# Optimization experiments

Measured on AMD Instinct MI355X. Metric: run time of the kernel, lower is better.

The kernel has to match this reference:

```python
import jax, jax.numpy as jnp
import numpy as np

INF = 10000.0


def setup_inputs() -> dict:
    key = jax.random.key(0)
    ks = jax.random.split(key, 4)
    bs, seqlen, hidden = 8, 512, 768
    head_size, heads = 64, 12
    inputs = jax.random.normal(ks[0], (bs, seqlen, hidden), dtype=jnp.float32)
    attention_mask = jnp.ones((bs, seqlen), dtype=jnp.int32)
    W1 = jax.random.normal(ks[1], (hidden, head_size * 2), dtype=jnp.float32) * 0.02
    b1 = jnp.zeros((head_size * 2,), dtype=jnp.float32)
    W2 = jax.random.normal(ks[2], (head_size * 2, heads * 2), dtype=jnp.float32) * 0.02
    b2 = jnp.zeros((heads * 2,), dtype=jnp.float32)
    return {"inputs": inputs, "attention_mask": attention_mask,
            "W1": W1, "b1": b1, "W2": W2, "b2": b2}


def _rope(t, sin, cos):
    # t: [b, s, d]; sin/cos: [s, d//2]
    t1, t2 = t[..., 0::2], t[..., 1::2]
    return jnp.stack([t1 * cos - t2 * sin, t1 * sin + t2 * cos], axis=-1).reshape(t.shape)


def reference(inputs, attention_mask, W1, b1, W2, b2):
    bs, seqlen = inputs.shape[:2]
    head_size = W1.shape[1] // 2
    x = inputs @ W1 + b1                      # [b, s, 2*head_size]
    qw, kw = x[..., 0::2], x[..., 1::2]       # [b, s, head_size] each
    # rotary embedding (computed like the buffer in the torch module)
    pos = jnp.arange(seqlen, dtype=jnp.float32)
    inv_freq = 1.0 / (10000.0 ** (jnp.arange(0, head_size, 2, dtype=jnp.float32) / head_size))
    freqs = pos[:, None] * inv_freq[None, :]  # [s, head_size//2]
    sin, cos = jnp.sin(freqs), jnp.cos(freqs)
    qw = _rope(qw, sin, cos)
    kw = _rope(kw, sin, cos)
    logits = jnp.einsum('bmd,bnd->bmn', qw, kw) / (head_size ** 0.5)  # [b, s, s]
    bias = (x @ W2 + b2).transpose(0, 2, 1) / 2.0                      # [b, 2*heads, s]
    logits = logits[:, None] + bias[:, ::2, None, :] + bias[:, 1::2, :, None]  # [b, h, s, s]
    am = attention_mask.astype(logits.dtype)
    mask = 1.0 - am[:, None, None, :] * am[:, None, :, None]           # [b, 1, s, s]
    logits = logits - mask * INF
    # tril mask: positions with end < start (j < i)
    idx = jnp.arange(seqlen)
    tril = (idx[None, :] < idx[:, None]).astype(logits.dtype)[None, None]  # [1, 1, s, s]
    logits = logits - tril * INF
    mask_out = jnp.logical_or(mask.astype(bool),
                              jnp.broadcast_to(tril.astype(bool), (bs, 1, seqlen, seqlen)))
    return logits, mask_out
```

## Files before the change

kernel.cpp:

```cpp
#include <hip/hip_runtime.h>

#define BSZ 8
#define SEQ 512
#define HID 768
#define N1 128
#define N2 24
#define HS 64
#define HEADS 12
#define INFV 10000.0f

typedef __attribute__((ext_vector_type(8))) short s8b;
typedef __attribute__((ext_vector_type(4))) float f32x4;

__device__ __forceinline__ unsigned short f2bf(float f) {
    union { float f; unsigned int u; } c; c.f = f;
    unsigned int u = c.u;
    u += 0x7FFFu + ((u >> 16) & 1u);
    return (unsigned short)(u >> 16);
}

__global__ __launch_bounds__(128) void k0_w1t(const float* __restrict__ W1,
                                              unsigned short* __restrict__ W1T) {
    const int c = threadIdx.x;
    const int k0 = blockIdx.x * 8;
    unsigned short v[8];
#pragma unroll
    for (int i = 0; i < 8; ++i)
        v[i] = f2bf(W1[(size_t)(k0 + i) * N1 + c]);
    unsigned short* dst = W1T + (size_t)c * HID + k0;
#pragma unroll
    for (int i = 0; i < 8; ++i) dst[i] = v[i];
}

__global__ __launch_bounds__(512, 2) void k1_proj(
    const float* __restrict__ inp, const unsigned short* __restrict__ W1T,
    const float* __restrict__ b1, const float* __restrict__ W2,
    const float* __restrict__ b2, float* __restrict__ qw,
    float* __restrict__ kwT, float* __restrict__ biasT)
{
    __shared__ unsigned short aF[96 * 16 * 8];
    __shared__ float xs[16 * N1];
    __shared__ float kT[HS][17];

    const int tid = threadIdx.x;
    const int row0 = blockIdx.x * 16;
    const int b = row0 >> 9;
    const int m0 = row0 & 511;

    {
        const float4* src = (const float4*)(inp + (size_t)row0 * HID);
#pragma unroll
        for (int i = 0; i < 6; ++i) {
            int f4 = tid + i * 512;
            int r = f4 / 192;
            int c4 = f4 % 192;
            float4 v = src[f4];
            int chunk = c4 >> 1;
            int half = c4 & 1;
            ushort4 w;
            w.x = f2bf(v.x); w.y = f2bf(v.y); w.z = f2bf(v.z); w.w = f2bf(v.w);
            *(ushort4*)&aF[(chunk * 16 + r) * 8 + half * 4] = w;
        }
    }
    __syncthreads();

    const int wv = tid >> 6;
    const int ln = tid & 63;
    const int lr = ln & 15;
    const int lg = ln >> 4;
    const int c0 = wv * 16;

    const s8b* bp = (const s8b*)W1T + ((size_t)(c0 + lr) * 96 + lg);

    f32x4 acc = {0.f, 0.f, 0.f, 0.f};
#pragma unroll
    for (int kc = 0; kc < 24; ++kc) {
        s8b a = *(const s8b*)&aF[((kc * 4 + lg) * 16 + lr) * 8];
        s8b bw = bp[kc * 4];
        acc = __builtin_amdgcn_mfma_f32_16x16x32_bf16(a, bw, acc, 0, 0, 0);
    }

    {
        float b1v = b1[c0 + lr];
#pragma unroll
        for (int g = 0; g < 4; ++g)
            xs[(lg * 4 + g) * N1 + c0 + lr] = acc[g] + b1v;
    }
    __syncthreads();

    {
        const int r = tid >> 5, j = tid & 31;
        const int m = m0 + r;
        const float C = 0.4152410118609203f;
        float invf = exp2f(-(float)j * C);
        float ang = (float)m * invf;
        float sv, cv;
        sincosf(ang, &sv, &cv);
        float4 xv = *(const float4*)&xs[r * N1 + 4 * j];
        float rq0 = xv.x * cv - xv.z * sv;
        float rq1 = xv.x * sv + xv.z * cv;
        float rk0 = xv.y * cv - xv.w * sv;
        float rk1 = xv.y * sv + xv.w * cv;
        *(float2*)(qw + (size_t)(b * SEQ + m) * HS + 2 * j) = make_float2(rq0, rq1);
        kT[2 * j][r]     = rk0;
        kT[2 * j + 1][r] = rk1;
    }
    if (tid < 16 * N2) {
        int r = tid / N2, c = tid - r * N2;
        const float* xr = &xs[r * N1];
        float dot = b2[c];
#pragma unroll 8
        for (int k = 0; k < N1; ++k)
            dot = fmaf(xr[k], W2[k * N2 + c], dot);
        biasT[(size_t)(b * N2 + c) * SEQ + m0 + r] = dot * 0.5f;
    }
    __syncthreads();

    {
        int d = tid >> 3, q = tid & 7;
        float2 v = *(const float2*)&kT[d][2 * q];
        *(float2*)(kwT + (size_t)(b * HS + d) * SEQ + m0 + 2 * q) = v;
    }
}

__global__ __launch_bounds__(256) void k2_out(
    const float* __restrict__ qw, const float* __restrict__ kwT,
    const float* __restrict__ biasT, const int* __restrict__ am,
    float* __restrict__ out)
{
    __shared__ float q_lds[8][HS];
    __shared__ float bo[8][HEADS];
    __shared__ int amm[8];

    const int tid = threadIdx.x;
    const int b = blockIdx.x >> 6;
    const int m0 = (blockIdx.x & 63) * 8;

#pragma unroll
    for (int i = 0; i < 2; ++i) {
        int idx = tid + i * 256;
        q_lds[idx >> 6][idx & 63] = qw[(size_t)(b * SEQ + m0) * HS + idx];
    }
    if (tid < 96) {
        int r = tid / 12, h = tid - r * 12;
        bo[r][h] = biasT[(size_t)(b * N2 + 2 * h + 1) * SEQ + m0 + r];
    }
    if (tid < 8) amm[tid] = am[b * SEQ + m0 + tid];
    __syncthreads();

    const int n0 = tid * 2;
    float qk0[8] = {0, 0, 0, 0, 0, 0, 0, 0};
    float qk1[8] = {0, 0, 0, 0, 0, 0, 0, 0};

#pragma unroll
    for (int dc = 0; dc < 2; ++dc) {
        float2 kn[32];
#pragma unroll
        for (int d = 0; d < 32; ++d)
            kn[d] = *(const float2*)&kwT[(size_t)(b * HS + dc * 32 + d) * SEQ + n0];
#pragma unroll
        for (int r = 0; r < 8; ++r) {
#pragma unroll
            for (int d4 = 0; d4 < 8; ++d4) {
                float4 qv = *(const float4*)&q_lds[r][dc * 32 + d4 * 4];
                qk0[r] = fmaf(qv.x, kn[d4 * 4 + 0].x, qk0[r]);
                qk0[r] = fmaf(qv.y, kn[d4 * 4 + 1].x, qk0[r]);
                qk0[r] = fmaf(qv.z, kn[d4 * 4 + 2].x, qk0[r]);
                qk0[r] = fmaf(qv.w, kn[d4 * 4 + 3].x, qk0[r]);
                qk1[r] = fmaf(qv.x, kn[d4 * 4 + 0].y, qk1[r]);
                qk1[r] = fmaf(qv.y, kn[d4 * 4 + 1].y, qk1[r]);
                qk1[r] = fmaf(qv.z, kn[d4 * 4 + 2].y, qk1[r]);
                qk1[r] = fmaf(qv.w, kn[d4 * 4 + 3].y, qk1[r]);
            }
        }
    }

    const int amn0 = am[b * SEQ + n0];
    const int amn1 = am[b * SEQ + n0 + 1];
    float pen0[8], pen1[8];
    float2 mo[8];
#pragma unroll
    for (int r = 0; r < 8; ++r) {
        int m = m0 + r;
        float msk0 = (1.0f - (float)(amn0 * amm[r])) * INFV;
        float msk1 = (1.0f - (float)(amn1 * amm[r])) * INFV;
        pen0[r] = msk0 + ((n0 < m) ? INFV : 0.0f);
        pen1[r] = msk1 + ((n0 + 1 < m) ? INFV : 0.0f);
        bool b0 = (amn0 * amm[r] != 1) || (n0 < m);
        bool b1m = (amn1 * amm[r] != 1) || (n0 + 1 < m);
        mo[r].x = b0 ? 1.0f : 0.0f;
        mo[r].y = b1m ? 1.0f : 0.0f;
    }

    float2 be[HEADS];
#pragma unroll
    for (int h = 0; h < HEADS; ++h)
        be[h] = *(const float2*)&biasT[(size_t)(b * N2 + 2 * h) * SEQ + n0];

    const size_t obase = (size_t)b * HEADS * SEQ * SEQ + n0;
#pragma unroll
    for (int h = 0; h < HEADS; ++h) {
#pragma unroll
        for (int r = 0; r < 8; ++r) {
            float2 v;
            v.x = fmaf(qk0[r], 0.125f, be[h].x + bo[r][h]) - pen0[r];
            v.y = fmaf(qk1[r], 0.125f, be[h].y + bo[r][h]) - pen1[r];
            *(float2*)&out[obase + ((size_t)h * SEQ + m0 + r) * SEQ] = v;
        }
    }
    const size_t mbase = (size_t)BSZ * HEADS * SEQ * SEQ
                       + ((size_t)b * SEQ + m0) * SEQ + n0;
#pragma unroll
    for (int r = 0; r < 8; ++r)
        *(float2*)&out[mbase + (size_t)r * SEQ] = mo[r];
}

extern "C" void kernel_launch(void* const* d_in, const int* in_sizes, int n_in,
                              void* d_out, int out_size, void* d_ws, size_t ws_size,
                              hipStream_t stream) {
    const float* inp = (const float*)d_in[0];
    const int*   am  = (const int*)d_in[1];
    const float* W1  = (const float*)d_in[2];
    const float* b1  = (const float*)d_in[3];
    const float* W2  = (const float*)d_in[4];
    const float* b2  = (const float*)d_in[5];

    float* ws    = (float*)d_ws;
    float* qw    = ws;
    float* kwT   = ws + 262144;
    float* biasT = ws + 524288;
    unsigned short* W1T = (unsigned short*)(ws + 622592);

    float* out = (float*)d_out;

    hipLaunchKernelGGL(k0_w1t, dim3(96), dim3(128), 0, stream, W1, W1T);
    hipLaunchKernelGGL(k1_proj, dim3(4096 / 16), dim3(512), 0, stream,
                       inp, W1T, b1, W2, b2, qw, kwT, biasT);
    hipLaunchKernelGGL(k2_out, dim3(4096 / 8), dim3(256), 0, stream,
                       qw, kwT, biasT, am, out);
}
```

Before: 48.23 us.

## Split projection kernel over column halves and precompute rope and W2 transpose

The projection kernel now runs twice as many blocks, each covering half of the 128 output columns. Within a block, the K dimension is split across two wave groups whose partial sums are reduced through shared memory. The W2 bias projection is split into two partial buffers that the output kernel adds back together. The prep kernel now also transposes W2 and builds a sin/cos table, which removes the per-block transcendental work. This targets poor parallelism in k1 (only 256 blocks), at the cost of re-converting the input to bf16 twice and extra bias reads in k2.

```diff
diff --git a/kernel.cpp b/kernel.cpp
--- a/kernel.cpp
+++ b/kernel.cpp
@@ -19,31 +19,58 @@
     return (unsigned short)(u >> 16);
 }
 
-__global__ __launch_bounds__(128) void k0_w1t(const float* __restrict__ W1,
-                                              unsigned short* __restrict__ W1T) {
-    const int c = threadIdx.x;
-    const int k0 = blockIdx.x * 8;
-    unsigned short v[8];
-#pragma unroll
-    for (int i = 0; i < 8; ++i)
-        v[i] = f2bf(W1[(size_t)(k0 + i) * N1 + c]);
-    unsigned short* dst = W1T + (size_t)c * HID + k0;
-#pragma unroll
-    for (int i = 0; i < 8; ++i) dst[i] = v[i];
-}
-
-__global__ __launch_bounds__(512, 2) void k1_proj(
+__global__ __launch_bounds__(128) void k0_prep(
+    const float* __restrict__ W1, const float* __restrict__ W2,
+    unsigned short* __restrict__ W1T, float* __restrict__ W2T,
+    float2* __restrict__ sct)
+{
+    const int tid = threadIdx.x;
+    const int bid = blockIdx.x;
+    if (bid < 96) {
+        const int c = tid;
+        const int k0 = bid * 8;
+        unsigned short v[8];
+#pragma unroll
+        for (int i = 0; i < 8; ++i)
+            v[i] = f2bf(W1[(size_t)(k0 + i) * N1 + c]);
+        unsigned short* dst = W1T + (size_t)c * HID + k0;
+#pragma unroll
+        for (int i = 0; i < 8; ++i) dst[i] = v[i];
+    } else if (bid == 96) {
+#pragma unroll
+        for (int c = 0; c < N2; ++c)
+            W2T[c * N1 + tid] = W2[tid * N2 + c];
+    } else {
+        const float C = 0.4152410118609203f;
+        int e0 = (bid - 97) * 512 + tid * 4;
+#pragma unroll
+        for (int u = 0; u < 4; ++u) {
+            int e = e0 + u;
+            int m = e >> 5, j = e & 31;
+            float ang = (float)m * exp2f(-(float)j * C);
+            float sv, cv;
+            sincosf(ang, &sv, &cv);
+            sct[e] = make_float2(sv, cv);
+        }
+    }
+}
+
+__global__ __launch_bounds__(512, 4) void k1_proj(
     const float* __restrict__ inp, const unsigned short* __restrict__ W1T,
-    const float* __restrict__ b1, const float* __restrict__ W2,
-    const float* __restrict__ b2, float* __restrict__ qw,
-    float* __restrict__ kwT, float* __restrict__ biasT)
+    const float* __restrict__ b1, const float* __restrict__ W2T,
+    const float* __restrict__ b2, const float2* __restrict__ sct,
+    float* __restrict__ qw, float* __restrict__ kwT,
+    float* __restrict__ bP0, float* __restrict__ bP1)
 {
     __shared__ unsigned short aF[96 * 16 * 8];
-    __shared__ float xs[16 * N1];
-    __shared__ float kT[HS][17];
+    __shared__ float ps[16][64];
+    __shared__ float xs[16][72];
+    __shared__ float kT[32][17];
 
     const int tid = threadIdx.x;
-    const int row0 = blockIdx.x * 16;
+    const int rt = blockIdx.x >> 1;
+    const int ch = blockIdx.x & 1;
+    const int row0 = rt * 16;
     const int b = row0 >> 9;
     const int m0 = row0 & 511;
 
@@ -68,65 +95,75 @@
     const int ln = tid & 63;
     const int lr = ln & 15;
     const int lg = ln >> 4;
-    const int c0 = wv * 16;
-
-    const s8b* bp = (const s8b*)W1T + ((size_t)(c0 + lr) * 96 + lg);
+    const int w3 = wv & 3;
+    const int kh = wv >> 2;
+    const int cg = ch * 64 + w3 * 16 + lr;
+
+    const s8b* bp = (const s8b*)W1T + ((size_t)cg * 96 + kh * 48 + lg);
 
     f32x4 acc = {0.f, 0.f, 0.f, 0.f};
 #pragma unroll
-    for (int kc = 0; kc < 24; ++kc) {
-        s8b a = *(const s8b*)&aF[((kc * 4 + lg) * 16 + lr) * 8];
-        s8b bw = bp[kc * 4];
-        acc = __builtin_amdgcn_mfma_f32_16x16x32_bf16(a, bw, acc, 0, 0, 0);
-    }
-
-    {
-        float b1v = b1[c0 + lr];
+    for (int kc = 0; kc < 12; ++kc) {
+        s8b a = *(const s8b*)&aF[(((kh * 12 + kc) * 4 + lg) * 16 + lr) * 8];
+        acc = __builtin_amdgcn_mfma_f32_16x16x32_bf16(a, bp[kc * 4], acc, 0, 0, 0);
+    }
+
+    if (kh == 1) {
+#pragma unroll
+        for (int g = 0; g < 4; ++g) ps[lg * 4 + g][w3 * 16 + lr] = acc[g];
+    }
+    __syncthreads();
+    if (kh == 0) {
+        float b1v = b1[cg];
 #pragma unroll
         for (int g = 0; g < 4; ++g)
-            xs[(lg * 4 + g) * N1 + c0 + lr] = acc[g] + b1v;
-    }
-    __syncthreads();
-
-    {
-        const int r = tid >> 5, j = tid & 31;
-        const int m = m0 + r;
-        const float C = 0.4152410118609203f;
-        float invf = exp2f(-(float)j * C);
-        float ang = (float)m * invf;
-        float sv, cv;
-        sincosf(ang, &sv, &cv);
-        float4 xv = *(const float4*)&xs[r * N1 + 4 * j];
-        float rq0 = xv.x * cv - xv.z * sv;
-        float rq1 = xv.x * sv + xv.z * cv;
-        float rk0 = xv.y * cv - xv.w * sv;
-        float rk1 = xv.y * sv + xv.w * cv;
-        *(float2*)(qw + (size_t)(b * SEQ + m) * HS + 2 * j) = make_float2(rq0, rq1);
-        kT[2 * j][r]     = rk0;
-        kT[2 * j + 1][r] = rk1;
-    }
+            xs[lg * 4 + g][w3 * 16 + lr] = acc[g] + ps[lg * 4 + g][w3 * 16 + lr] + b1v;
+    }
+    __syncthreads();
+
     if (tid < 16 * N2) {
         int r = tid / N2, c = tid - r * N2;
-        const float* xr = &xs[r * N1];
-        float dot = b2[c];
-#pragma unroll 8
-        for (int k = 0; k < N1; ++k)
-            dot = fmaf(xr[k], W2[k * N2 + c], dot);
-        biasT[(size_t)(b * N2 + c) * SEQ + m0 + r] = dot * 0.5f;
-    }
-    __syncthreads();
-
-    {
-        int d = tid >> 3, q = tid & 7;
-        float2 v = *(const float2*)&kT[d][2 * q];
-        *(float2*)(kwT + (size_t)(b * HS + d) * SEQ + m0 + 2 * q) = v;
+        const float* xr = &xs[r][0];
+        const float* wr = W2T + c * N1 + ch * 64;
+        float dot = (ch == 0) ? b2[c] : 0.0f;
+#pragma unroll
+        for (int k4 = 0; k4 < 16; ++k4) {
+            float4 xv = *(const float4*)&xr[k4 * 4];
+            float4 wv2 = *(const float4*)&wr[k4 * 4];
+            dot = fmaf(xv.x, wv2.x, dot); dot = fmaf(xv.y, wv2.y, dot);
+            dot = fmaf(xv.z, wv2.z, dot); dot = fmaf(xv.w, wv2.w, dot);
+        }
+        float* bP = ch ? bP1 : bP0;
+        bP[(size_t)(b * N2 + c) * SEQ + m0 + r] = dot * 0.5f;
+    }
+
+    if (tid < 256) {
+        const int r = tid >> 4, jj = tid & 15;
+        const int j = ch * 16 + jj;
+        const int m = m0 + r;
+        float2 sc = sct[m * 32 + j];
+        float4 xv = *(const float4*)&xs[r][4 * jj];
+        float rq0 = xv.x * sc.y - xv.z * sc.x;
+        float rq1 = xv.x * sc.x + xv.z * sc.y;
+        float rk0 = xv.y * sc.y - xv.w * sc.x;
+        float rk1 = xv.y * sc.x + xv.w * sc.y;
+        *(float2*)(qw + (size_t)(b * SEQ + m) * HS + 2 * j) = make_float2(rq0, rq1);
+        kT[2 * jj][r]     = rk0;
+        kT[2 * jj + 1][r] = rk1;
+    }
+    __syncthreads();
+
+    if (tid < 256) {
+        int dl = tid >> 3, q = tid & 7;
+        float2 v = *(const float2*)&kT[dl][2 * q];
+        *(float2*)(kwT + (size_t)(b * HS + ch * 32 + dl) * SEQ + m0 + 2 * q) = v;
     }
 }
 
 __global__ __launch_bounds__(256) void k2_out(
     const float* __restrict__ qw, const float* __restrict__ kwT,
-    const float* __restrict__ biasT, const int* __restrict__ am,
-    float* __restrict__ out)
+    const float* __restrict__ bP0, const float* __restrict__ bP1,
+    const int* __restrict__ am, float* __restrict__ out)
 {
     __shared__ float q_lds[8][HS];
     __shared__ float bo[8][HEADS];
@@ -143,7 +180,8 @@
     }
     if (tid < 96) {
         int r = tid / 12, h = tid - r * 12;
-        bo[r][h] = biasT[(size_t)(b * N2 + 2 * h + 1) * SEQ + m0 + r];
+        size_t ix = (size_t)(b * N2 + 2 * h + 1) * SEQ + m0 + r;
+        bo[r][h] = bP0[ix] + bP1[ix];
     }
     if (tid < 8) amm[tid] = am[b * SEQ + m0 + tid];
     __syncthreads();
@@ -194,8 +232,12 @@
 
     float2 be[HEADS];
 #pragma unroll
-    for (int h = 0; h < HEADS; ++h)
-        be[h] = *(const float2*)&biasT[(size_t)(b * N2 + 2 * h) * SEQ + n0];
+    for (int h = 0; h < HEADS; ++h) {
+        size_t ix = (size_t)(b * N2 + 2 * h) * SEQ + n0;
+        float2 e0 = *(const float2*)&bP0[ix];
+        float2 e1 = *(const float2*)&bP1[ix];
+        be[h] = make_float2(e0.x + e1.x, e0.y + e1.y);
+    }
 
     const size_t obase = (size_t)b * HEADS * SEQ * SEQ + n0;
 #pragma unroll
@@ -228,14 +270,18 @@
     float* ws    = (float*)d_ws;
     float* qw    = ws;
     float* kwT   = ws + 262144;
-    float* biasT = ws + 524288;
-    unsigned short* W1T = (unsigned short*)(ws + 622592);
+    float* bP0   = ws + 524288;
+    float* bP1   = ws + 622592;
+    unsigned short* W1T = (unsigned short*)(ws + 720896);
+    float* W2T   = ws + 819200;
+    float2* sct  = (float2*)(ws + 822272);
 
     float* out = (float*)d_out;
 
-    hipLaunchKernelGGL(k0_w1t, dim3(96), dim3(128), 0, stream, W1, W1T);
-    hipLaunchKernelGGL(k1_proj, dim3(4096 / 16), dim3(512), 0, stream,
-                       inp, W1T, b1, W2, b2, qw, kwT, biasT);
+    hipLaunchKernelGGL(k0_prep, dim3(129), dim3(128), 0, stream,
+                       W1, W2, W1T, W2T, sct);
+    hipLaunchKernelGGL(k1_proj, dim3(512), dim3(512), 0, stream,
+                       inp, W1T, b1, W2T, b2, sct, qw, kwT, bP0, bP1);
     hipLaunchKernelGGL(k2_out, dim3(4096 / 8), dim3(256), 0, stream,
-                       qw, kwT, biasT, am, out);
-}
+                       qw, kwT, bP0, bP1, am, out);
+}
```

Result: slower. 49.84 us (+3.3%).
